# Kernel optimization log

Hardware: AMD Instinct MI355X
Metric: run time of the kernel (lower is better)

The kernel has to match this reference:

```python
import jax, jax.numpy as jnp
import numpy as np

N, E, G, L, D = 50000, 800000, 512, 3, 128
BN_EPS = 1e-5


def setup_inputs() -> dict:
    key = jax.random.key(0)
    ks = jax.random.split(key, 16)
    x = jax.random.normal(ks[0], (N, D), dtype=jnp.float32)
    edge_index = jax.random.randint(ks[1], (2, E), 0, N)
    batch = jnp.sort(jax.random.randint(ks[2], (N,), 0, G))
    W1 = jax.random.normal(ks[3], (L, D, D), dtype=jnp.float32) * 0.05
    b1 = jax.random.normal(ks[4], (L, D), dtype=jnp.float32) * 0.05
    gamma = jax.random.uniform(ks[5], (L, D), dtype=jnp.float32) + 0.5
    beta = jax.random.normal(ks[6], (L, D), dtype=jnp.float32) * 0.05
    running_mean = jax.random.normal(ks[7], (L, D), dtype=jnp.float32) * 0.1
    running_var = jax.random.uniform(ks[8], (L, D), dtype=jnp.float32) + 0.5
    W2 = jax.random.normal(ks[9], (L, D, D), dtype=jnp.float32) * 0.05
    b2 = jax.random.normal(ks[10], (L, D), dtype=jnp.float32) * 0.05
    lin1_W = jax.random.normal(ks[11], (L * D, L * D), dtype=jnp.float32) * 0.05
    lin1_b = jax.random.normal(ks[12], (L * D,), dtype=jnp.float32) * 0.05
    lin2_W = jax.random.normal(ks[13], (L * D, 10), dtype=jnp.float32) * 0.05
    lin2_b = jax.random.normal(ks[14], (10,), dtype=jnp.float32) * 0.05
    return {"x": x, "edge_index": edge_index, "batch": batch,
            "W1": W1, "b1": b1, "gamma": gamma, "beta": beta,
            "running_mean": running_mean, "running_var": running_var,
            "W2": W2, "b2": b2, "lin1_W": lin1_W, "lin1_b": lin1_b,
            "lin2_W": lin2_W, "lin2_b": lin2_b}


def _gin_layer(h, src, dst, W1, b1, gamma, beta, rm, rv, W2, b2):
    # GINConv (eps=0): MLP((1+eps)*x + sum_{j->i} x_j); aggregate src->dst
    agg = jax.ops.segment_sum(h[src], dst, num_segments=N)  # [N, D]
    z = (h + agg) @ W1 + b1
    # BatchNorm1d in eval mode (running stats)
    z = (z - rm) * (gamma / jnp.sqrt(rv + BN_EPS)) + beta
    z = jax.nn.relu(z)
    return jax.nn.relu(z @ W2 + b2)


def reference(x, edge_index, batch, W1, b1, gamma, beta, running_mean,
              running_var, W2, b2, lin1_W, lin1_b, lin2_W, lin2_b):
    src, dst = edge_index[0], edge_index[1]
    h = x
    pooled = []
    for i in range(L):
        h = _gin_layer(h, src, dst, W1[i], b1[i], gamma[i], beta[i],
                       running_mean[i], running_var[i], W2[i], b2[i])
        pooled.append(jax.ops.segment_sum(h, batch, num_segments=G))  # [G, D]
    g = jnp.concatenate(pooled, axis=1)  # [G, L*D]
    g = jax.nn.relu(g @ lin1_W + lin1_b)
    # dropout is identity in eval mode
    return g @ lin2_W + lin2_b  # [G, num_classes]
```

## Files before the change

kernel.cpp:

```cpp
#include <hip/hip_runtime.h>
#include <hip/hip_bf16.h>

#define D_FEAT 128
#define N_GRAPHS 512
#define N_LAYERS 3
#define POOL_DIM (N_LAYERS * D_FEAT)
#define N_CLASSES 10
#define BN_EPS 1e-5f
#define CAP 64
#define NBINS 8
#define SLABCAP 768
#define NSLICE 4


typedef __attribute__((ext_vector_type(8))) short bf16x8;
typedef __attribute__((ext_vector_type(8))) unsigned short ushort8;
typedef __attribute__((ext_vector_type(4))) float f32x4;

__device__ __forceinline__ unsigned short f2bf(float f) {
    unsigned u = __builtin_bit_cast(unsigned, f);
    u += 0x7FFFu + ((u >> 16) & 1u);
    return (unsigned short)(u >> 16);
}
__device__ __forceinline__ float bf2f(unsigned short h) {
    unsigned u = ((unsigned)h) << 16;
    return __builtin_bit_cast(float, u);
}
__device__ __forceinline__ float bf_lo(unsigned u) {
    return __builtin_bit_cast(float, u << 16);
}
__device__ __forceinline__ float bf_hi(unsigned u) {
    return __builtin_bit_cast(float, u & 0xffff0000u);
}

__global__ __launch_bounds__(256) void setup_kernel(
        const float* __restrict__ x, unsigned short* __restrict__ xb,
        const float* __restrict__ W1, const float* __restrict__ W2,
        unsigned short* __restrict__ Wt,
        const float* __restrict__ b1, const float* __restrict__ gamma,
        const float* __restrict__ beta, const float* __restrict__ rm,
        const float* __restrict__ rv, const float* __restrict__ b2,
        float* __restrict__ ea, float* __restrict__ eb,
        int* __restrict__ cursor, float* __restrict__ pooled,
        const int* __restrict__ ei, int2* __restrict__ pairs,
        int* __restrict__ cnts, int E,
        int N, int n4, int B0, int B1, int B2, int B3, int B4) {
    int b = blockIdx.x, tid = threadIdx.x;
    if (b < B0) {
        int i = b * 256 + tid;
        if (i < n4) {
            float4 v = ((const float4*)x)[i];
            ushort4 o;
            o.x = f2bf(v.x); o.y = f2bf(v.y); o.z = f2bf(v.z); o.w = f2bf(v.w);
            int node = i >> 5;
            int c4 = i & 31;
            int sl = c4 >> 3;
            int off = c4 & 7;
            ((ushort4*)xb)[((size_t)sl * N + node) * 8 + off] = o;
        }
    } else if (b < B1) {
        __shared__ float tile[64][65];
        int t = b - B0;
        int slot = t >> 2;
        int r0 = ((t >> 1) & 1) * 64;
        int c0 = (t & 1) * 64;
        int l = slot >> 1;
        const float* W = (slot & 1) ? W2 : W1;
        const float* Wb = W + (size_t)l * D_FEAT * D_FEAT;
        int rr = tid >> 2, cc4 = (tid & 3) * 16;
        #pragma unroll
        for (int j = 0; j < 16; ++j)
            tile[rr][cc4 + j] = Wb[(size_t)(r0 + rr) * D_FEAT + c0 + cc4 + j];
        __syncthreads();
        int nn = tid >> 2, kk4 = (tid & 3) * 16;
        unsigned short* Wo = Wt + (size_t)slot * D_FEAT * D_FEAT;
        #pragma unroll
        for (int j = 0; j < 16; ++j)
            Wo[(size_t)(c0 + nn) * D_FEAT + r0 + kk4 + j] = f2bf(tile[kk4 + j][nn]);
    } else if (b < B2) {
        int i = (b - B1) * 256 + tid;
        if (i < N_LAYERS * D_FEAT) {
            int l = i >> 7, c = i & 127;
            float s = gamma[i] * rsqrtf(rv[i] + BN_EPS);
            ea[(2 * l) * D_FEAT + c] = s;
            eb[(2 * l) * D_FEAT + c] = (b1[i] - rm[i]) * s + beta[i];
            ea[(2 * l + 1) * D_FEAT + c] = 1.0f;
            eb[(2 * l + 1) * D_FEAT + c] = b2[i];
        }
    } else if (b < B3) {
        int i = (b - B2) * 256 + tid;
        if (i < N) cursor[i] = 0;
    } else if (b < B4) {
        int i = (b - B3) * 256 + tid;
        if (i < N_GRAPHS * POOL_DIM) pooled[i] = 0.f;
    } else {
        __shared__ int loc[NBINS];
        int bb = b - B4;
        int per = (E + 255) / 256;
        int e0 = bb * per;
        int e1 = e0 + per; if (e1 > E) e1 = E;
        int span = (N + NBINS - 1) / NBINS;
        if (tid < NBINS) loc[tid] = 0;
        __syncthreads();
        for (int e = e0 + tid; e < e1; e += 256) {
            int dst = ei[E + e];
            int src = ei[e];
            int bin = dst / span;
            int p = atomicAdd(&loc[bin], 1);
            if (p < SLABCAP)
                pairs[((size_t)(bin * 256 + bb)) * SLABCAP + p] = make_int2(src, dst);
        }
        __syncthreads();
        if (tid < NBINS)
            cnts[tid * 256 + bb] = loc[tid];
    }
}

__global__ __launch_bounds__(256) void fill_v3(const int2* __restrict__ pairs,
                                               const int* __restrict__ cnts,
                                               int* __restrict__ cursor,
                                               unsigned short* __restrict__ bucket) {
    int r = blockIdx.x & 7;
    int chunk = blockIdx.x >> 3;
    #pragma unroll
    for (int s = 0; s < 4; ++s) {
        int blk = chunk * 4 + s;
        int cnt = cnts[r * 256 + blk];
        if (cnt > SLABCAP) cnt = SLABCAP;
        const int2* slab = pairs + (size_t)(r * 256 + blk) * SLABCAP;
        for (int p = threadIdx.x; p < cnt; p += 256) {
            int2 pr = slab[p];
            int pos = atomicAdd(&cursor[pr.y], 1);
            if (pos < CAP)
                bucket[(size_t)pr.y * CAP + pos] = (unsigned short)pr.x;
        }
    }
}

__global__ __launch_bounds__(256) void agg_slice(
        const unsigned short* __restrict__ hs,
        const int* __restrict__ deg,
        const unsigned short* __restrict__ bucket,
        unsigned short* __restrict__ ys,
        int n, int nchunks) {
    int xcd = blockIdx.x & 7;
    int s = xcd >> 1;
    int worker = (blockIdx.x >> 3) * 2 + (xcd & 1);
    int wave = threadIdx.x >> 6, lane = threadIdx.x & 63;
    int grp = lane >> 2, sub = lane & 3;
    const uint4* h4 = (const uint4*)hs;
    size_t sbase = (size_t)s * n * 4;

    for (int chunk = worker; chunk < nchunks; chunk += 512) {
        int n0 = chunk * 64 + wave * 16 + grp;
        bool valid = n0 < n;
        int node = valid ? n0 : 0;
        int d = valid ? deg[node] : 0;
        if (d > CAP) d = CAP;
        const unsigned short* brow = bucket + (size_t)node * CAP;

        uint4 iv = *(const uint4*)&brow[sub * 8];

        uint4 sv = h4[sbase + (size_t)node * 4 + sub];

        int dmax = d;
        dmax = max(dmax, __shfl_xor(dmax, 4));
        dmax = max(dmax, __shfl_xor(dmax, 8));
        dmax = max(dmax, __shfl_xor(dmax, 16));
        dmax = max(dmax, __shfl_xor(dmax, 32));

        float acc[8] = {0.f,0.f,0.f,0.f,0.f,0.f,0.f,0.f};

        auto do4 = [&](int e0, unsigned q0, unsigned q1) {
            int id[4];
            id[0] = (int)(q0 & 0xffffu);
            id[1] = (int)(q0 >> 16);
            id[2] = (int)(q1 & 0xffffu);
            id[3] = (int)(q1 >> 16);
            uint4 w[4];
            #pragma unroll
            for (int u = 0; u < 4; ++u) {
                w[u] = make_uint4(0u, 0u, 0u, 0u);
                if (e0 + u < d)
                    w[u] = h4[sbase + (size_t)id[u] * 4 + sub];
            }
            #pragma unroll
            for (int u = 0; u < 4; ++u) {
                uint4 v = w[u];
                acc[0] += bf_lo(v.x); acc[1] += bf_hi(v.x);
                acc[2] += bf_lo(v.y); acc[3] += bf_hi(v.y);
                acc[4] += bf_lo(v.z); acc[5] += bf_hi(v.z);
                acc[6] += bf_lo(v.w); acc[7] += bf_hi(v.w);
            }
        };

        int dcap = dmax < 32 ? dmax : 32;
        for (int t = 0; t < dcap; t += 8) {
            int src = (grp << 2) + (t >> 3);
            unsigned q0 = (unsigned)__shfl((int)iv.x, src);
            unsigned q1 = (unsigned)__shfl((int)iv.y, src);
            do4(t, q0, q1);
            q0 = (unsigned)__shfl((int)iv.z, src);
            q1 = (unsigned)__shfl((int)iv.w, src);
            do4(t + 4, q0, q1);
        }
        for (int e = 32; e < d; ++e) {
            int idx = (int)brow[e];
            uint4 v = h4[sbase + (size_t)idx * 4 + sub];
            acc[0] += bf_lo(v.x); acc[1] += bf_hi(v.x);
            acc[2] += bf_lo(v.y); acc[3] += bf_hi(v.y);
            acc[4] += bf_lo(v.z); acc[5] += bf_hi(v.z);
            acc[6] += bf_lo(v.w); acc[7] += bf_hi(v.w);
        }

        acc[0] += bf_lo(sv.x); acc[1] += bf_hi(sv.x);
        acc[2] += bf_lo(sv.y); acc[3] += bf_hi(sv.y);
        acc[4] += bf_lo(sv.z); acc[5] += bf_hi(sv.z);
        acc[6] += bf_lo(sv.w); acc[7] += bf_hi(sv.w);

        if (valid) {
            uint4 o;
            o.x = (unsigned)f2bf(acc[0]) | ((unsigned)f2bf(acc[1]) << 16);
            o.y = (unsigned)f2bf(acc[2]) | ((unsigned)f2bf(acc[3]) << 16);
            o.z = (unsigned)f2bf(acc[4]) | ((unsigned)f2bf(acc[5]) << 16);
            o.w = (unsigned)f2bf(acc[6]) | ((unsigned)f2bf(acc[7]) << 16);
            ((uint4*)ys)[sbase + (size_t)node * 4 + sub] = o;
        }
    }
}

__global__ __launch_bounds__(256) void layer_fused(const unsigned short* __restrict__ A,
                                                   const unsigned short* __restrict__ Wt1,
                                                   const unsigned short* __restrict__ Wt2,
                                                   const float* __restrict__ ea1,
                                                   const float* __restrict__ eb1,
                                                   const float* __restrict__ ea2,
                                                   const float* __restrict__ eb2,
                                                   const int* __restrict__ batch,
                                                   float* __restrict__ pooled, int loff,
                                                   unsigned short* __restrict__ outh, int n) {
    __shared__ unsigned short As[64][136];
    __shared__ unsigned short Ws[128][136];
    int tid = threadIdx.x;
    int row0 = blockIdx.x * 64;
    int wave = tid >> 6, lane = tid & 63;
    int m0 = wave * 16;
    int lrow = lane & 15, lq = lane >> 4;

    #pragma unroll
    for (int i = 0; i < 4; ++i) {
        int idx = tid + i * 256;
        int r = idx >> 4, c = (idx & 15) * 8;
        int sl = c >> 5, off = c & 31;
        ushort8 v = (ushort8)0;
        if (row0 + r < n)
            v = *(const ushort8*)&A[((size_t)sl * n + (row0 + r)) * 32 + off];
        *(ushort8*)&As[r][c] = v;
    }
    #pragma unroll
    for (int i = 0; i < 8; ++i) {
        int idx = tid + i * 256;
        int r = idx >> 4, c = (idx & 15) * 8;
        *(ushort8*)&Ws[r][c] = *(const ushort8*)&Wt1[(size_t)r * D_FEAT + c];
    }

    ushort8 w2reg[8];
    #pragma unroll
    for (int i = 0; i < 8; ++i) {
        int idx = tid + i * 256;
        int r = idx >> 4, c = (idx & 15) * 8;
        w2reg[i] = *(const ushort8*)&Wt2[(size_t)r * D_FEAT + c];
    }

    int gr0 = row0 + m0 + lq * 4;
    int bq[4];
    if (gr0 + 3 < n) {
        int4 b4 = *(const int4*)&batch[gr0];
        bq[0] = b4.x; bq[1] = b4.y; bq[2] = b4.z; bq[3] = b4.w;
    } else {
        #pragma unroll
        for (int r = 0; r < 4; ++r)
            bq[r] = (gr0 + r < n) ? batch[gr0 + r] : -1;
    }
    __syncthreads();

    f32x4 acc[8] = {};
    #pragma unroll
    for (int t = 0; t < 4; ++t) {
        bf16x8 a = *(const bf16x8*)&As[m0 + lrow][t * 32 + lq * 8];
        #pragma unroll
        for (int nt = 0; nt < 8; ++nt) {
            bf16x8 b = *(const bf16x8*)&Ws[nt * 16 + lrow][t * 32 + lq * 8];
            acc[nt] = __builtin_amdgcn_mfma_f32_16x16x32_bf16(a, b, acc[nt], 0, 0, 0);
        }
    }
    __syncthreads();

    #pragma unroll
    for (int nt = 0; nt < 8; ++nt) {
        int col = nt * 16 + lrow;
        float al = ea1[col], be = eb1[col];
        #pragma unroll
        for (int r = 0; r < 4; ++r) {
            float v = fmaxf(fmaf(acc[nt][r], al, be), 0.f);
            As[m0 + lq * 4 + r][col] = f2bf(v);
        }
    }
    #pragma unroll
    for (int i = 0; i < 8; ++i) {
        int idx = tid + i * 256;
        int r = idx >> 4, c = (idx & 15) * 8;
        *(ushort8*)&Ws[r][c] = w2reg[i];
    }
    __syncthreads();

    f32x4 acc2[8] = {};
    #pragma unroll
    for (int t = 0; t < 4; ++t) {
        bf16x8 a = *(const bf16x8*)&As[m0 + lrow][t * 32 + lq * 8];
        #pragma unroll
        for (int nt = 0; nt < 8; ++nt) {
            bf16x8 b = *(const bf16x8*)&Ws[nt * 16 + lrow][t * 32 + lq * 8];
            acc2[nt] = __builtin_amdgcn_mfma_f32_16x16x32_bf16(a, b, acc2[nt], 0, 0, 0);
        }
    }

    float vv[8][4];
    #pragma unroll
    for (int nt = 0; nt < 8; ++nt) {
        int col = nt * 16 + lrow;
        float al = ea2[col], be = eb2[col];
        int sl = col >> 5, off = col & 31;
        #pragma unroll
        for (int r = 0; r < 4; ++r) {
            unsigned short hb = f2bf(fmaxf(fmaf(acc2[nt][r], al, be), 0.f));
            vv[nt][r] = bf2f(hb);
            if (outh) {
                int grow = row0 + m0 + lq * 4 + r;
                if (grow < n)
                    outh[((size_t)sl * n + grow) * 32 + off] = hb;
            }
        }
    }

    int gmn = 0x7fffffff, gmx = -1;
    #pragma unroll
    for (int r = 0; r < 4; ++r) {
        if (bq[r] >= 0) {
            gmn = bq[r] < gmn ? bq[r] : gmn;
            gmx = bq[r] > gmx ? bq[r] : gmx;
        }
    }
    {
        int t;
        t = __shfl_xor(gmn, 16); gmn = t < gmn ? t : gmn;
        t = __shfl_xor(gmn, 32); gmn = t < gmn ? t : gmn;
        t = __shfl_xor(gmx, 16); gmx = t > gmx ? t : gmx;
        t = __shfl_xor(gmx, 32); gmx = t > gmx ? t : gmx;
    }
    for (int seg = gmn; seg <= gmx; ++seg) {
        #pragma unroll
        for (int nt = 0; nt < 8; ++nt) {
            float s = 0.f;
            #pragma unroll
            for (int r = 0; r < 4; ++r)
                if (bq[r] == seg) s += vv[nt][r];
            s += __shfl_xor(s, 16);
            s += __shfl_xor(s, 32);
            if (lq == 0 && s != 0.f)
                atomicAdd(&pooled[(size_t)seg * POOL_DIM + loff + nt * 16 + lrow], s);
        }
    }
}

__global__ __launch_bounds__(384) void head_kernel(const float* __restrict__ pooled,
                                                   const float* __restrict__ W1,
                                                   const float* __restrict__ b1v,
                                                   const float* __restrict__ W2,
                                                   const float* __restrict__ b2v,
                                                   float* __restrict__ out) {
    __shared__ float f1[4][POOL_DIM];
    int j = threadIdx.x;
    int g0 = blockIdx.x * 4;
    const float* pr = pooled + (size_t)g0 * POOL_DIM;
    float bb = b1v[j];
    float s0 = bb, s1 = bb, s2 = bb, s3 = bb;
    for (int k0 = 0; k0 < POOL_DIM; k0 += 8) {
        float w[8];
        #pragma unroll
        for (int i = 0; i < 8; ++i)
            w[i] = W1[(size_t)(k0 + i) * POOL_DIM + j];
        #pragma unroll
        for (int i = 0; i < 8; ++i) {
            int k = k0 + i;
            s0 = fmaf(pr[k],                w[i], s0);
            s1 = fmaf(pr[POOL_DIM + k],     w[i], s1);
            s2 = fmaf(pr[2 * POOL_DIM + k], w[i], s2);
            s3 = fmaf(pr[3 * POOL_DIM + k], w[i], s3);
        }
    }
    f1[0][j] = fmaxf(s0, 0.f);
    f1[1][j] = fmaxf(s1, 0.f);
    f1[2][j] = fmaxf(s2, 0.f);
    f1[3][j] = fmaxf(s3, 0.f);
    __syncthreads();
    if (j < 4 * N_CLASSES) {
        int g = j / N_CLASSES, c = j % N_CLASSES;
        float s = b2v[c];
        for (int k = 0; k < POOL_DIM; ++k)
            s = fmaf(f1[g][k], W2[(size_t)k * N_CLASSES + c], s);
        out[(size_t)(g0 + g) * N_CLASSES + c] = s;
    }
}

extern "C" void kernel_launch(void* const* d_in, const int* in_sizes, int n_in,
                              void* d_out, int out_size, void* d_ws, size_t ws_size,
                              hipStream_t stream) {
    const float* x      = (const float*)d_in[0];
    const int*   ei     = (const int*)  d_in[1];
    const int*   batch  = (const int*)  d_in[2];
    const float* W1     = (const float*)d_in[3];
    const float* b1     = (const float*)d_in[4];
    const float* gamma  = (const float*)d_in[5];
    const float* beta   = (const float*)d_in[6];
    const float* rm     = (const float*)d_in[7];
    const float* rv     = (const float*)d_in[8];
    const float* W2     = (const float*)d_in[9];
    const float* b2     = (const float*)d_in[10];
    const float* lin1W  = (const float*)d_in[11];
    const float* lin1b  = (const float*)d_in[12];
    const float* lin2W  = (const float*)d_in[13];
    const float* lin2b  = (const float*)d_in[14];
    float* out = (float*)d_out;

    const int N = in_sizes[0] / D_FEAT;
    const int E = in_sizes[1] / 2;

    char* ws = (char*)d_ws;
    auto carve = [&](size_t bytes) {
        char* p = ws;
        ws += (bytes + 255) & ~(size_t)255;
        return p;
    };
    int*   cursor    = (int*)  carve((size_t)N * 4);
    int*   cnts      = (int*)  carve((size_t)NBINS * 256 * 4);
    unsigned short* bucket = (unsigned short*)carve((size_t)N * CAP * 2);
    int2*  pairs     = (int2*) carve((size_t)NBINS * 256 * SLABCAP * 8);
    float* ea        = (float*)carve((size_t)2 * N_LAYERS * D_FEAT * 4);
    float* eb        = (float*)carve((size_t)2 * N_LAYERS * D_FEAT * 4);
    unsigned short* Wt   = (unsigned short*)carve((size_t)2 * N_LAYERS * D_FEAT * D_FEAT * 2);
    unsigned short* xb   = (unsigned short*)carve((size_t)N * D_FEAT * 2);
    unsigned short* ybuf = (unsigned short*)carve((size_t)N * D_FEAT * 2);
    unsigned short* hbuf = (unsigned short*)carve((size_t)N * D_FEAT * 2);
    float* pooled    = (float*)carve((size_t)N_GRAPHS * POOL_DIM * 4);

    const int n4 = N * D_FEAT / 4;
    const int B0 = (n4 + 255) / 256;
    const int B1 = B0 + 24;
    const int B2 = B1 + 2;
    const int B3 = B2 + (N + 255) / 256;
    const int B4 = B3 + (N_GRAPHS * POOL_DIM + 255) / 256;
    const int B5 = B4 + 256;

    setup_kernel<<<B5, 256, 0, stream>>>(x, xb, W1, W2, Wt, b1, gamma, beta,
                                         rm, rv, b2, ea, eb, cursor, pooled,
                                         ei, pairs, cnts, E,
                                         N, n4, B0, B1, B2, B3, B4);
    fill_v3<<<8 * 64, 256, 0, stream>>>(pairs, cnts, cursor, bucket);

    const int nchunks = (N + 63) / 64;

    const unsigned short* hprev = xb;
    for (int l = 0; l < N_LAYERS; ++l) {
        agg_slice<<<2048, 256, 0, stream>>>(hprev, cursor, bucket, ybuf,
                                            N, nchunks);
        unsigned short* outh = (l == N_LAYERS - 1) ? nullptr : hbuf;
        layer_fused<<<(N + 63) / 64, 256, 0, stream>>>(ybuf,
                      Wt + (size_t)(2 * l) * D_FEAT * D_FEAT,
                      Wt + (size_t)(2 * l + 1) * D_FEAT * D_FEAT,
                      ea + (size_t)(2 * l) * D_FEAT,
                      eb + (size_t)(2 * l) * D_FEAT,
                      ea + (size_t)(2 * l + 1) * D_FEAT,
                      eb + (size_t)(2 * l + 1) * D_FEAT,
                      batch, pooled, l * D_FEAT, outh, N);
        hprev = hbuf;
    }
    head_kernel<<<N_GRAPHS / 4, 384, 0, stream>>>(pooled, lin1W, lin1b, lin2W, lin2b, out);
}
```

Measured before the change: 304.4 us.

## Sort nodes by degree to balance aggregation work across wave lanes

```diff
diff --git a/kernel.cpp b/kernel.cpp
--- a/kernel.cpp
+++ b/kernel.cpp
@@ -41,7 +41,8 @@
         const float* __restrict__ beta, const float* __restrict__ rm,
         const float* __restrict__ rv, const float* __restrict__ b2,
         float* __restrict__ ea, float* __restrict__ eb,
-        int* __restrict__ cursor, float* __restrict__ pooled,
+        int* __restrict__ cursor, int* __restrict__ hist,
+        float* __restrict__ pooled,
         const int* __restrict__ ei, int2* __restrict__ pairs,
         int* __restrict__ cnts, int E,
         int N, int n4, int B0, int B1, int B2, int B3, int B4) {
@@ -90,6 +91,7 @@
     } else if (b < B3) {
         int i = (b - B2) * 256 + tid;
         if (i < N) cursor[i] = 0;
+        if (b == B2 && tid <= CAP) hist[tid] = 0;
     } else if (b < B4) {
         int i = (b - B3) * 256 + tid;
         if (i < N_GRAPHS * POOL_DIM) pooled[i] = 0.f;
@@ -137,9 +139,59 @@
     }
 }
 
+__global__ __launch_bounds__(256) void hist_kernel(const int* __restrict__ deg,
+                                                   int* __restrict__ hist, int n) {
+    __shared__ int lh[CAP + 1];
+    int tid = threadIdx.x;
+    if (tid <= CAP) lh[tid] = 0;
+    __syncthreads();
+    int i = blockIdx.x * 256 + tid;
+    if (i < n) {
+        int d = deg[i]; if (d > CAP) d = CAP;
+        atomicAdd(&lh[d], 1);
+    }
+    __syncthreads();
+    if (tid <= CAP && lh[tid] > 0) atomicAdd(&hist[tid], lh[tid]);
+}
+
+__global__ __launch_bounds__(64) void scan_kernel(int* __restrict__ hist) {
+    if (threadIdx.x == 0) {
+        int acc = 0;
+        for (int d = 0; d <= CAP; ++d) { int c = hist[d]; hist[d] = acc; acc += c; }
+    }
+}
+
+__global__ __launch_bounds__(256) void scatter_kernel(const int* __restrict__ deg,
+                                                      int* __restrict__ base,
+                                                      int* __restrict__ perm,
+                                                      int* __restrict__ degp, int n) {
+    __shared__ int lh[CAP + 1];
+    __shared__ int lb[CAP + 1];
+    int tid = threadIdx.x;
+    if (tid <= CAP) lh[tid] = 0;
+    __syncthreads();
+    int i = blockIdx.x * 256 + tid;
+    int d = -1;
+    if (i < n) { d = deg[i]; if (d > CAP) d = CAP; atomicAdd(&lh[d], 1); }
+    __syncthreads();
+    if (tid <= CAP) {
+        int c = lh[tid];
+        lb[tid] = c > 0 ? atomicAdd(&base[tid], c) : 0;
+        lh[tid] = 0;
+    }
+    __syncthreads();
+    if (i < n) {
+        int p = atomicAdd(&lh[d], 1);
+        int pos = lb[d] + p;
+        perm[pos] = i;
+        degp[pos] = d;
+    }
+}
+
 __global__ __launch_bounds__(256) void agg_slice(
         const unsigned short* __restrict__ hs,
-        const int* __restrict__ deg,
+        const int* __restrict__ degp,
+        const int* __restrict__ perm,
         const unsigned short* __restrict__ bucket,
         unsigned short* __restrict__ ys,
         int n, int nchunks) {
@@ -152,11 +204,10 @@
     size_t sbase = (size_t)s * n * 4;
 
     for (int chunk = worker; chunk < nchunks; chunk += 512) {
-        int n0 = chunk * 64 + wave * 16 + grp;
-        bool valid = n0 < n;
-        int node = valid ? n0 : 0;
-        int d = valid ? deg[node] : 0;
-        if (d > CAP) d = CAP;
+        int jj = chunk * 64 + wave * 16 + grp;
+        bool valid = jj < n;
+        int node = 0, d = 0;
+        if (valid) { node = perm[jj]; d = degp[jj]; }
         const unsigned short* brow = bucket + (size_t)node * CAP;
 
         uint4 iv = *(const uint4*)&brow[sub * 8];
@@ -453,6 +504,9 @@
     unsigned short* ybuf = (unsigned short*)carve((size_t)N * D_FEAT * 2);
     unsigned short* hbuf = (unsigned short*)carve((size_t)N * D_FEAT * 2);
     float* pooled    = (float*)carve((size_t)N_GRAPHS * POOL_DIM * 4);
+    int*   hist      = (int*)  carve((size_t)(CAP + 1) * 4);
+    int*   perm      = (int*)  carve((size_t)N * 4);
+    int*   degp      = (int*)  carve((size_t)N * 4);
 
     const int n4 = N * D_FEAT / 4;
     const int B0 = (n4 + 255) / 256;
@@ -463,16 +517,21 @@
     const int B5 = B4 + 256;
 
     setup_kernel<<<B5, 256, 0, stream>>>(x, xb, W1, W2, Wt, b1, gamma, beta,
-                                         rm, rv, b2, ea, eb, cursor, pooled,
-                                         ei, pairs, cnts, E,
+                                         rm, rv, b2, ea, eb, cursor, hist,
+                                         pooled, ei, pairs, cnts, E,
                                          N, n4, B0, B1, B2, B3, B4);
     fill_v3<<<8 * 64, 256, 0, stream>>>(pairs, cnts, cursor, bucket);
 
+    const int sblocks = (N + 255) / 256;
+    hist_kernel<<<sblocks, 256, 0, stream>>>(cursor, hist, N);
+    scan_kernel<<<1, 64, 0, stream>>>(hist);
+    scatter_kernel<<<sblocks, 256, 0, stream>>>(cursor, hist, perm, degp, N);
+
     const int nchunks = (N + 63) / 64;
 
     const unsigned short* hprev = xb;
     for (int l = 0; l < N_LAYERS; ++l) {
-        agg_slice<<<2048, 256, 0, stream>>>(hprev, cursor, bucket, ybuf,
+        agg_slice<<<2048, 256, 0, stream>>>(hprev, degp, perm, bucket, ybuf,
                                             N, nchunks);
         unsigned short* outh = (l == N_LAYERS - 1) ? nullptr : hbuf;
         layer_fused<<<(N + 63) / 64, 256, 0, stream>>>(ybuf,
```

Result: slower. 317.8 us (+4.4%).
